# Kernel tuning notes

Hardware: AMD Instinct MI355X
Metric: run time of the kernel (lower is better)

Reference implementation:

```python
import jax, jax.numpy as jnp
import numpy as np

N_LEVELS = 16
N_FEATS = 2
MIN_RES = 16
MAX_RES = 2048
LOG2_T = 19
T = 1 << LOG2_T  # 524288 hash-table entries per level
B = np.exp((np.log(MAX_RES) - np.log(MIN_RES)) / (N_LEVELS - 1))  # per-level scale ~1.3819
PRIME_Y = np.uint32(2654435761)  # tcnn 2D spatial-hash prime (x prime is 1)
MASK = jnp.uint32(T - 1)


def hash_encode(uv, table):
    """Multiresolution hash-grid encoding (tcnn HashGrid, 2D, bilinear).
    uv: [N,2] in [0,1); table: [L,T,F]. Returns [N, L*F]."""
    outs = []
    for l in range(N_LEVELS):
        scale = MIN_RES * (B ** l) - 1.0          # tcnn grid_scale
        res = int(np.ceil(scale)) + 1             # tcnn grid_resolution
        dense = (res * res) <= T                  # small levels are dense grids
        pos = uv * jnp.float32(scale) + jnp.float32(0.5)
        pg_f = jnp.floor(pos)
        frac = pos - pg_f                          # [N,2] bilinear weights
        pg = pg_f.astype(jnp.uint32)

        def corner_idx(ox, oy):
            x = pg[:, 0] + jnp.uint32(ox)
            y = pg[:, 1] + jnp.uint32(oy)
            if dense:
                return (x + y * jnp.uint32(res)) & MASK
            return (x ^ (y * PRIME_Y)) & MASK

        fx = frac[:, 0:1]
        fy = frac[:, 1:2]
        tl = table[l]
        feat = ((1.0 - fx) * (1.0 - fy) * tl[corner_idx(0, 0)]
                + fx * (1.0 - fy) * tl[corner_idx(1, 0)]
                + (1.0 - fx) * fy * tl[corner_idx(0, 1)]
                + fx * fy * tl[corner_idx(1, 1)])
        outs.append(feat)
    return jnp.concatenate(outs, axis=-1)  # [N, 32]


def mlp(x, w0, w1, w2):
    # FullyFusedMLP: no biases, ReLU hidden, Sigmoid output
    h = jax.nn.relu(x @ w0)
    h = jax.nn.relu(h @ w1)
    return jax.nn.sigmoid(h @ w2)  # [N, 3]


def setup_inputs() -> dict:
    key = jax.random.key(0)
    ks = jax.random.split(key, 5)
    N = 2_097_152
    uv = jax.random.uniform(ks[0], (N, 2), jnp.float32)
    # tcnn HashGrid init: uniform in [-1e-4, 1e-4]
    table = jax.random.uniform(ks[1], (N_LEVELS, T, N_FEATS), jnp.float32, -1e-4, 1e-4)
    w0 = jax.random.normal(ks[2], (32, 64), jnp.float32) * jnp.float32(1.0 / np.sqrt(32))
    w1 = jax.random.normal(ks[3], (64, 64), jnp.float32) * jnp.float32(1.0 / np.sqrt(64))
    w2 = jax.random.normal(ks[4], (64, 3), jnp.float32) * jnp.float32(1.0 / np.sqrt(64))
    return {"uv": uv, "table": table, "w0": w0, "w1": w1, "w2": w2}


def reference(uv, table, w0, w1, w2):
    return mlp(hash_encode(uv, table), w0, w1, w2)
```

## Files before the change

### kernel.cpp

```cpp
#include <hip/hip_runtime.h>
#include <math.h>
#include <stdint.h>

#define NLV 16
#define LOG2T 19
#define TSZ (1u << LOG2T)
#define TMASK (TSZ - 1u)
#define PRIME_Y 2654435761u

#define WP8_BYTES  (4 * 64 * 8)
#define WP16_BYTES (10 * 64 * 16)
#define WPF_BYTES  (WP8_BYTES + WP16_BYTES)

#define FSCALE 8192.0f
#define FUNSCALE (1.0f / 8192.0f)

#define NCOARSE 512
#define P1_PTS 8192
#define P2_CAP 5120

struct NGPParams {
    float scale[NLV];
    unsigned res[NLV];
    unsigned hashed_mask;
};

struct __align__(8) pairld { float x, y, z, w; };

typedef __attribute__((ext_vector_type(8))) short bf16x8;
typedef __attribute__((ext_vector_type(4))) float f32x4;

__device__ inline ushort bf16_rn(float f) {
    uint32_t u = __float_as_uint(f);
    return (ushort)((u + 0x7FFFu + ((u >> 16) & 1u)) >> 16);
}
__device__ inline uint32_t pack_trunc(float a, float b) {
    return __builtin_amdgcn_perm(__float_as_uint(a), __float_as_uint(b), 0x07060302u);
}
__device__ inline ushort cvt_pk_fp8(float a, float b) {
    unsigned r = 0;
    asm("v_cvt_pk_fp8_f32 %0, %1, %2" : "+v"(r) : "v"(a), "v"(b));
    return (ushort)r;
}
__device__ inline unsigned coarse_of(float2 v) {
    unsigned b = (unsigned)(v.y * 512.f); return b > 511u ? 511u : b;
}
__device__ inline unsigned fine_of(float2 v) {
    unsigned b = (unsigned)(v.x * 256.f); return b > 255u ? 255u : b;
}
__device__ inline int xcd_swz(int orig, int nwg) {
    const int q = nwg >> 3, r = nwg & 7;
    const int xcd = orig & 7, k = orig >> 3;
    return (xcd < r ? xcd * (q + 1) : r * (q + 1) + (xcd - r) * q) + k;
}

__global__ __launch_bounds__(256) void ngp_prep_wfrag(
    const float* __restrict__ w0, const float* __restrict__ w1,
    const float* __restrict__ w2,
    unsigned long long* __restrict__ wp8, ushort* __restrict__ wp16,
    uint32_t* __restrict__ hist)
{
    const int t = threadIdx.x;
    hist[t] = 0; hist[t + 256] = 0;
    {
        const int f = t >> 6, lane = t & 63;
        const int g4 = lane >> 4, r16 = lane & 15;
        const int nn = f * 16 + r16, k0 = 8 * g4;
        float v[8];
        #pragma unroll
        for (int j = 0; j < 8; ++j) v[j] = w0[(k0 + j) * 64 + nn];
        const unsigned long long p0 = cvt_pk_fp8(v[0], v[1]);
        const unsigned long long p1 = cvt_pk_fp8(v[2], v[3]);
        const unsigned long long p2 = cvt_pk_fp8(v[4], v[5]);
        const unsigned long long p3 = cvt_pk_fp8(v[6], v[7]);
        wp8[f * 64 + lane] = p0 | (p1 << 16) | (p2 << 32) | (p3 << 48);
    }
    for (int i = 0; i < 3; ++i) {
        const int e = t + 256 * i;
        if (e >= 640) continue;
        const int f = e >> 6, lane = e & 63;
        const int g4 = lane >> 4, r16 = lane & 15;
        ushort v[8];
        if (f < 8) {
            const int nn = (f >> 1) * 16 + r16, k0 = (f & 1) * 32 + 8 * g4;
            #pragma unroll
            for (int j = 0; j < 8; ++j) v[j] = bf16_rn(w1[(k0 + j) * 64 + nn]);
        } else {
            const int nn = r16, k0 = (f - 8) * 32 + 8 * g4;
            #pragma unroll
            for (int j = 0; j < 8; ++j)
                v[j] = (nn < 3) ? bf16_rn(w2[(k0 + j) * 3 + nn]) : (ushort)0;
        }
        #pragma unroll
        for (int j = 0; j < 8; ++j) wp16[e * 8 + j] = v[j];
    }
}

__global__ __launch_bounds__(1024) void ngp_hist512(
    const float2* __restrict__ uv, uint32_t* __restrict__ hist, int n)
{
    __shared__ unsigned int h[NCOARSE];
    const int t = threadIdx.x;
    if (t < NCOARSE) h[t] = 0;
    __syncthreads();
    const int b0 = blockIdx.x * P1_PTS;
    #pragma unroll
    for (int k = 0; k < 8; ++k) {
        const int i = b0 + t + k * 1024;
        if (i < n) atomicAdd(&h[coarse_of(uv[i])], 1u);
    }
    __syncthreads();
    if (t < NCOARSE && h[t]) atomicAdd(&hist[t], h[t]);
}

__global__ __launch_bounds__(512) void ngp_scan512(
    const uint32_t* __restrict__ hist, uint32_t* __restrict__ base,
    uint32_t* __restrict__ cursor)
{
    __shared__ unsigned int s[NCOARSE];
    const int t = threadIdx.x;
    const uint32_t mine = hist[t];
    s[t] = mine;
    __syncthreads();
    for (int off = 1; off < NCOARSE; off <<= 1) {
        uint32_t v = (t >= off) ? s[t - off] : 0u;
        __syncthreads();
        s[t] += v;
        __syncthreads();
    }
    const uint32_t excl = s[t] - mine;
    base[t] = excl;
    cursor[t] = excl;
}

__global__ __launch_bounds__(1024) void ngp_pass1(
    const float2* __restrict__ uv, uint32_t* __restrict__ cursor,
    float2* __restrict__ suv, uint32_t* __restrict__ perm, int n)
{
    __shared__ float2       spt[P1_PTS];
    __shared__ unsigned int sid[P1_PTS];
    __shared__ unsigned int hist[NCOARSE], lbase[NCOARSE], lcur[NCOARSE], gbase[NCOARSE];
    __shared__ unsigned int stot;

    const int t = threadIdx.x;
    const int b0 = blockIdx.x * P1_PTS;
    if (t < NCOARSE) hist[t] = 0;
    __syncthreads();

    float2 p[8]; unsigned pc[8];
    #pragma unroll
    for (int k = 0; k < 8; ++k) {
        const int i = b0 + t + k * 1024;
        if (i < n) {
            p[k] = uv[i];
            pc[k] = coarse_of(p[k]);
            atomicAdd(&hist[pc[k]], 1u);
        } else pc[k] = 0xFFFFFFFFu;
    }
    __syncthreads();
    if (t < NCOARSE) lbase[t] = hist[t];
    __syncthreads();
    for (int off = 1; off < NCOARSE; off <<= 1) {
        uint32_t v = 0;
        if (t < NCOARSE && t >= off) v = lbase[t - off];
        __syncthreads();
        if (t < NCOARSE) lbase[t] += v;
        __syncthreads();
    }
    if (t < NCOARSE) {
        const uint32_t excl = lbase[t] - hist[t];
        lcur[t] = excl;
        gbase[t] = atomicAdd(&cursor[t], hist[t]);
        lbase[t] = excl;
        if (t == NCOARSE - 1) stot = excl + hist[t];
    }
    __syncthreads();
    #pragma unroll
    for (int k = 0; k < 8; ++k) {
        if (pc[k] != 0xFFFFFFFFu) {
            const uint32_t r = atomicAdd(&lcur[pc[k]], 1u);
            spt[r] = p[k];
            sid[r] = (unsigned)(b0 + t + k * 1024);
        }
    }
    __syncthreads();
    const uint32_t tot = stot;
    for (uint32_t j = t; j < tot; j += 1024) {
        const float2 v = spt[j];
        const unsigned c = coarse_of(v);
        const uint32_t d = gbase[c] + (j - lbase[c]);
        suv[d] = v;
        perm[d] = sid[j];
    }
}

__global__ __launch_bounds__(1024) void ngp_pass2(
    const uint32_t* __restrict__ basev, const uint32_t* __restrict__ histv,
    float2* __restrict__ suv, uint32_t* __restrict__ perm)
{
    __shared__ float2       spt[P2_CAP];
    __shared__ unsigned int sid[P2_CAP];
    __shared__ unsigned int hist[256], lbase[256], lcur[256];

    const int b = blockIdx.x;
    const uint32_t lo = basev[b];
    const uint32_t cnt = histv[b];
    if (cnt > P2_CAP) return;
    const int t = threadIdx.x;
    if (t < 256) hist[t] = 0;
    __syncthreads();
    for (uint32_t j = t; j < cnt; j += 1024) {
        const float2 v = suv[lo + j];
        spt[j] = v; sid[j] = perm[lo + j];
        atomicAdd(&hist[fine_of(v)], 1u);
    }
    __syncthreads();
    if (t < 256) lbase[t] = hist[t];
    __syncthreads();
    for (int off = 1; off < 256; off <<= 1) {
        uint32_t v = 0;
        if (t < 256 && t >= off) v = lbase[t - off];
        __syncthreads();
        if (t < 256) lbase[t] += v;
        __syncthreads();
    }
    if (t < 256) lcur[t] = lbase[t] - hist[t];
    __syncthreads();
    for (uint32_t j = t; j < cnt; j += 1024) {
        const float2 v = spt[j];
        const uint32_t r = atomicAdd(&lcur[fine_of(v)], 1u);
        suv[lo + r] = v;
        perm[lo + r] = sid[j];
    }
}

__global__ __launch_bounds__(256) void ngp_encode2_kernel(
    const float2* __restrict__ pts,
    const float2* __restrict__ table,
    ushort* __restrict__ xt,
    NGPParams p, int n, int chunks2)
{
    const int bid = blockIdx.x;
    const int pass = bid / chunks2;
    const int chunk = xcd_swz(bid - pass * chunks2, chunks2);
    const int base = chunk * 512 + threadIdx.x;

    float2 xy[2];
    #pragma unroll
    for (int q = 0; q < 2; ++q) {
        int idx = base + q * 256;
        xy[q] = pts[idx < n ? idx : (n - 1)];
    }

    const int l0 = (pass == 0) ? 0 : (pass == 1 ? 10 : 10 + pass);
    const int l1 = (pass == 0) ? 9 : (pass == 1 ? 11 : 10 + pass);

    for (int l = l0; l <= l1; ++l) {
        const float s = p.scale[l];
        const unsigned res = p.res[l];
        const bool hashed = (p.hashed_mask >> l) & 1u;
        const float2* tl = table + ((size_t)l << LOG2T);

        #pragma unroll
        for (int q = 0; q < 2; ++q) {
            const float px = xy[q].x * s + 0.5f;
            const float py = xy[q].y * s + 0.5f;
            const float fpx = floorf(px), fpy = floorf(py);
            const float fx = px - fpx, fy = py - fpy;
            const unsigned x0 = (unsigned)fpx, y0 = (unsigned)fpy;

            float2 c00, c10, c01, c11;
            if (!hashed) {
                const unsigned b0 = x0 + y0 * res;
                const pairld q0 = *(const pairld*)(tl + b0);
                const pairld q1 = *(const pairld*)(tl + b0 + res);
                c00 = make_float2(q0.x, q0.y); c10 = make_float2(q0.z, q0.w);
                c01 = make_float2(q1.x, q1.y); c11 = make_float2(q1.z, q1.w);
            } else {
                const unsigned hy0 = y0 * PRIME_Y;
                const unsigned hy1 = (y0 + 1u) * PRIME_Y;
                if (!(x0 & 1u)) {
                    const unsigned i0 = (x0 ^ hy0) & TMASK;
                    const unsigned i2 = (x0 ^ hy1) & TMASK;
                    const pairld q0 = *(const pairld*)(tl + (i0 & ~1u));
                    const pairld q2 = *(const pairld*)(tl + (i2 & ~1u));
                    if (i0 & 1u) { c00 = make_float2(q0.z, q0.w); c10 = make_float2(q0.x, q0.y); }
                    else         { c00 = make_float2(q0.x, q0.y); c10 = make_float2(q0.z, q0.w); }
                    if (i2 & 1u) { c01 = make_float2(q2.z, q2.w); c11 = make_float2(q2.x, q2.y); }
                    else         { c01 = make_float2(q2.x, q2.y); c11 = make_float2(q2.z, q2.w); }
                } else {
                    c00 = tl[(x0 ^ hy0) & TMASK];
                    c10 = tl[((x0 + 1u) ^ hy0) & TMASK];
                    c01 = tl[(x0 ^ hy1) & TMASK];
                    c11 = tl[((x0 + 1u) ^ hy1) & TMASK];
                }
            }

            const float w00 = (1.f - fx) * (1.f - fy);
            const float w10 = fx * (1.f - fy);
            const float w01 = (1.f - fx) * fy;
            const float w11 = fx * fy;
            const float f0 = w00 * c00.x + w10 * c10.x + w01 * c01.x + w11 * c11.x;
            const float f1 = w00 * c00.y + w10 * c10.y + w01 * c01.y + w11 * c11.y;
            const ushort pk = cvt_pk_fp8(f0 * FSCALE, f1 * FSCALE);
            const int idx = base + q * 256;
            if (idx < n) xt[(size_t)l * n + idx] = pk;
        }
    }
}

__global__ __launch_bounds__(256, 4) void ngp_mlp_persist(
    const ushort* __restrict__ xt,
    const unsigned long long* __restrict__ wp8,
    const ushort* __restrict__ wp16,
    const uint32_t* __restrict__ perm,
    float* __restrict__ out, int n, int nchunks)
{
    __shared__ __align__(16) ushort H[256 * 72];

    const int t = threadIdx.x;
    const int lane = t & 63;
    const int w = t >> 6;
    const int g4 = lane >> 4;
    const int r16 = lane & 15;

    unsigned long long wf8[4];
    #pragma unroll
    for (int f = 0; f < 4; ++f) wf8[f] = wp8[f * 64 + lane];
    bf16x8 wf16[10];
    #pragma unroll
    for (int f = 0; f < 10; ++f)
        wf16[f] = *(const bf16x8*)(wp16 + (size_t)(f * 64 + lane) * 8);

    for (int c = blockIdx.x; c < nchunks; c += gridDim.x) {
        const int pbase = c << 8;
        #pragma unroll
        for (int mi = 0; mi < 4; ++mi) {
            const int plocal = (w * 4 + mi) * 16 + r16;
            int pg = pbase + plocal;
            pg = pg < n ? pg : n - 1;
            union { ushort s[4]; unsigned long long v; } xv;
            #pragma unroll
            for (int c4 = 0; c4 < 4; ++c4)
                xv.s[c4] = xt[(size_t)(4 * g4 + c4) * n + pg];
            f32x4 a[4];
            #pragma unroll
            for (int nt = 0; nt < 4; ++nt)
                a[nt] = __builtin_amdgcn_mfma_f32_16x16x32_fp8_fp8(
                    (long)wf8[nt], (long)xv.v, (f32x4){0.f, 0.f, 0.f, 0.f}, 0, 0, 0);
            const int pl = plocal * 72;
            #pragma unroll
            for (int nt = 0; nt < 4; ++nt) {
                const uint32_t d0 = pack_trunc(fmaxf(a[nt][1] * FUNSCALE, 0.f),
                                               fmaxf(a[nt][0] * FUNSCALE, 0.f));
                const uint32_t d1 = pack_trunc(fmaxf(a[nt][3] * FUNSCALE, 0.f),
                                               fmaxf(a[nt][2] * FUNSCALE, 0.f));
                *(uint2*)&H[pl + nt * 16 + 4 * g4] = make_uint2(d0, d1);
            }
        }
        #pragma unroll
        for (int mi = 0; mi < 4; ++mi) {
            const int plocal = (w * 4 + mi) * 16 + r16;
            const int pl = plocal * 72;
            const bf16x8 bh0 = *(const bf16x8*)&H[pl + 8 * g4];
            const bf16x8 bh1 = *(const bf16x8*)&H[pl + 32 + 8 * g4];
            #pragma unroll
            for (int nt = 0; nt < 4; ++nt) {
                f32x4 acc = __builtin_amdgcn_mfma_f32_16x16x32_bf16(
                    wf16[nt * 2], bh0, (f32x4){0.f, 0.f, 0.f, 0.f}, 0, 0, 0);
                acc = __builtin_amdgcn_mfma_f32_16x16x32_bf16(
                    wf16[nt * 2 + 1], bh1, acc, 0, 0, 0);
                const uint32_t d0 = pack_trunc(fmaxf(acc[1], 0.f), fmaxf(acc[0], 0.f));
                const uint32_t d1 = pack_trunc(fmaxf(acc[3], 0.f), fmaxf(acc[2], 0.f));
                *(uint2*)&H[pl + nt * 16 + 4 * g4] = make_uint2(d0, d1);
            }
            const bf16x8 ch0 = *(const bf16x8*)&H[pl + 8 * g4];
            const bf16x8 ch1 = *(const bf16x8*)&H[pl + 32 + 8 * g4];
            f32x4 z = __builtin_amdgcn_mfma_f32_16x16x32_bf16(
                wf16[8], ch0, (f32x4){0.f, 0.f, 0.f, 0.f}, 0, 0, 0);
            z = __builtin_amdgcn_mfma_f32_16x16x32_bf16(wf16[9], ch1, z, 0, 0, 0);
            if (g4 == 0) {
                const int pgs = pbase + plocal;
                if (pgs < n) {
                    const int pg = perm ? (int)perm[pgs] : pgs;
                    #pragma unroll
                    for (int r = 0; r < 3; ++r)
                        out[(size_t)pg * 3 + r] = 1.f / (1.f + __expf(-z[r]));
                }
            }
        }
    }
}

__global__ __launch_bounds__(256) void ngp_fused_kernel(
    const float2* __restrict__ uv,
    const float2* __restrict__ table,
    const float4* __restrict__ w0,
    const float4* __restrict__ w1,
    const float*  __restrict__ w2,
    float* __restrict__ out,
    NGPParams p, int n)
{
    __shared__ float4 sw0[512];
    __shared__ float4 sw1[1024];
    __shared__ float  sw2[192];
    const int t = threadIdx.x;
    #pragma unroll
    for (int i = 0; i < 2; i++) sw0[t + 256 * i] = w0[t + 256 * i];
    #pragma unroll
    for (int i = 0; i < 4; i++) sw1[t + 256 * i] = w1[t + 256 * i];
    if (t < 192) sw2[t] = w2[t];
    __syncthreads();
    const int gi = blockIdx.x * 256 + t;
    if (gi >= n) return;
    const float2 xy = uv[gi];
    float feat[32];
    #pragma unroll
    for (int l = 0; l < NLV; l++) {
        const float s = p.scale[l];
        const unsigned res = p.res[l];
        const float px = xy.x * s + 0.5f;
        const float py = xy.y * s + 0.5f;
        const float fpx = floorf(px), fpy = floorf(py);
        const float fx = px - fpx, fy = py - fpy;
        const unsigned x0 = (unsigned)fpx, y0 = (unsigned)fpy;
        unsigned i00, i10, i01, i11;
        if (!((p.hashed_mask >> l) & 1u)) {
            const unsigned b = x0 + y0 * res;
            i00 = b & TMASK; i10 = (b + 1u) & TMASK;
            i01 = (b + res) & TMASK; i11 = (b + res + 1u) & TMASK;
        } else {
            const unsigned hy0 = y0 * PRIME_Y;
            const unsigned hy1 = (y0 + 1u) * PRIME_Y;
            i00 = (x0 ^ hy0) & TMASK; i10 = ((x0 + 1u) ^ hy0) & TMASK;
            i01 = (x0 ^ hy1) & TMASK; i11 = ((x0 + 1u) ^ hy1) & TMASK;
        }
        const float2* tl = table + ((size_t)l << LOG2T);
        const float2 c00 = tl[i00], c10 = tl[i10], c01 = tl[i01], c11 = tl[i11];
        const float w00 = (1.f - fx) * (1.f - fy);
        const float w10 = fx * (1.f - fy);
        const float w01 = (1.f - fx) * fy;
        const float w11 = fx * fy;
        feat[2 * l]     = w00 * c00.x + w10 * c10.x + w01 * c01.x + w11 * c11.x;
        feat[2 * l + 1] = w00 * c00.y + w10 * c10.y + w01 * c01.y + w11 * c11.y;
    }
    float2 h0[32];
    #pragma unroll
    for (int j = 0; j < 32; j++) h0[j] = make_float2(0.f, 0.f);
    #pragma unroll
    for (int k = 0; k < 32; k++) {
        const float f = feat[k];
        #pragma unroll
        for (int j = 0; j < 16; j++) {
            const float4 ww = sw0[k * 16 + j];
            h0[2 * j].x = fmaf(f, ww.x, h0[2 * j].x);
            h0[2 * j].y = fmaf(f, ww.y, h0[2 * j].y);
            h0[2 * j + 1].x = fmaf(f, ww.z, h0[2 * j + 1].x);
            h0[2 * j + 1].y = fmaf(f, ww.w, h0[2 * j + 1].y);
        }
    }
    #pragma unroll
    for (int j = 0; j < 32; j++) {
        h0[j].x = fmaxf(h0[j].x, 0.f);
        h0[j].y = fmaxf(h0[j].y, 0.f);
    }
    float2 h1[32];
    #pragma unroll
    for (int j = 0; j < 32; j++) h1[j] = make_float2(0.f, 0.f);
    #pragma unroll
    for (int k = 0; k < 64; k++) {
        const float f = (k & 1) ? h0[k >> 1].y : h0[k >> 1].x;
        #pragma unroll
        for (int j = 0; j < 16; j++) {
            const float4 ww = sw1[k * 16 + j];
            h1[2 * j].x = fmaf(f, ww.x, h1[2 * j].x);
            h1[2 * j].y = fmaf(f, ww.y, h1[2 * j].y);
            h1[2 * j + 1].x = fmaf(f, ww.z, h1[2 * j + 1].x);
            h1[2 * j + 1].y = fmaf(f, ww.w, h1[2 * j + 1].y);
        }
    }
    #pragma unroll
    for (int j = 0; j < 32; j++) {
        h1[j].x = fmaxf(h1[j].x, 0.f);
        h1[j].y = fmaxf(h1[j].y, 0.f);
    }
    float z0 = 0.f, z1 = 0.f, z2 = 0.f;
    #pragma unroll
    for (int k = 0; k < 64; k++) {
        const float f = (k & 1) ? h1[k >> 1].y : h1[k >> 1].x;
        z0 = fmaf(f, sw2[3 * k + 0], z0);
        z1 = fmaf(f, sw2[3 * k + 1], z1);
        z2 = fmaf(f, sw2[3 * k + 2], z2);
    }
    out[3 * gi + 0] = 1.f / (1.f + __expf(-z0));
    out[3 * gi + 1] = 1.f / (1.f + __expf(-z1));
    out[3 * gi + 2] = 1.f / (1.f + __expf(-z2));
}

extern "C" void kernel_launch(void* const* d_in, const int* in_sizes, int n_in,
                              void* d_out, int out_size, void* d_ws, size_t ws_size,
                              hipStream_t stream) {
    const float2* uv    = (const float2*)d_in[0];
    const float2* table = (const float2*)d_in[1];
    const float*  w0f   = (const float*)d_in[2];
    const float*  w1f   = (const float*)d_in[3];
    const float*  w2f   = (const float*)d_in[4];
    float* out = (float*)d_out;

    const int n = in_sizes[0] / 2;

    NGPParams p;
    p.hashed_mask = 0;
    const double B = exp((log(2048.0) - log(16.0)) / 15.0);
    for (int l = 0; l < NLV; l++) {
        const double scale = 16.0 * pow(B, (double)l) - 1.0;
        const long long res = (long long)ceil(scale) + 1;
        p.scale[l] = (float)scale;
        p.res[l] = (unsigned)res;
        if (res * res > (long long)TSZ) p.hashed_mask |= (1u << l);
    }

    const size_t xt_bytes   = (size_t)NLV * (size_t)n * 2u;
    const size_t wpf_bytes  = ((size_t)WPF_BYTES + 63u) & ~63ull;
    const size_t suv_bytes  = (size_t)n * 8u;
    const size_t perm_bytes = (size_t)n * 4u;
    const size_t ctl_bytes  = (size_t)NCOARSE * 4u * 3u;

    const size_t need_sorted = xt_bytes + wpf_bytes + suv_bytes + perm_bytes + ctl_bytes;
    const size_t need_plain  = xt_bytes + wpf_bytes;

    const int chunks  = (n + 255) / 256;
    const int chunks2 = (n + 511) / 512;

    if (ws_size < need_plain) {
        ngp_fused_kernel<<<chunks, 256, 0, stream>>>(
            uv, table, (const float4*)w0f, (const float4*)w1f, w2f, out, p, n);
        return;
    }

    ushort* xt = (ushort*)d_ws;
    unsigned long long* wp8 = (unsigned long long*)((char*)d_ws + xt_bytes);
    ushort* wp16 = (ushort*)((char*)d_ws + xt_bytes + WP8_BYTES);

    float2*   suv    = (float2*)((char*)d_ws + xt_bytes + wpf_bytes);
    uint32_t* perm   = (uint32_t*)((char*)suv + suv_bytes);
    uint32_t* hist   = (uint32_t*)((char*)perm + perm_bytes);
    uint32_t* basev  = hist + NCOARSE;
    uint32_t* cursor = basev + NCOARSE;

    const int mlp_blocks = chunks < 1024 ? chunks : 1024;

    if (ws_size < need_sorted) {
        ngp_prep_wfrag<<<1, 256, 0, stream>>>(w0f, w1f, w2f, wp8, wp16,
                                              (uint32_t*)((char*)d_ws + xt_bytes + WPF_BYTES - 2048));
        ngp_encode2_kernel<<<6 * chunks2, 256, 0, stream>>>(uv, table, xt, p, n, chunks2);
        ngp_mlp_persist<<<mlp_blocks, 256, 0, stream>>>(xt, wp8, wp16,
                                                        (const uint32_t*)nullptr, out, n, chunks);
        return;
    }

    const int p1_blocks = (n + P1_PTS - 1) / P1_PTS;

    ngp_prep_wfrag<<<1, 256, 0, stream>>>(w0f, w1f, w2f, wp8, wp16, hist);
    ngp_hist512<<<p1_blocks, 1024, 0, stream>>>(uv, hist, n);
    ngp_scan512<<<1, NCOARSE, 0, stream>>>(hist, basev, cursor);
    ngp_pass1<<<p1_blocks, 1024, 0, stream>>>(uv, cursor, suv, perm, n);
    ngp_pass2<<<NCOARSE, 1024, 0, stream>>>(basev, hist, suv, perm);
    ngp_encode2_kernel<<<6 * chunks2, 256, 0, stream>>>(suv, table, xt, p, n, chunks2);
    ngp_mlp_persist<<<mlp_blocks, 256, 0, stream>>>(xt, wp8, wp16, perm, out, n, chunks);
}
```

Before: 172.6 us.

## Fold global scan into sort passes and merge encode level passes

```diff
diff --git a/kernel.cpp b/kernel.cpp
--- a/kernel.cpp
+++ b/kernel.cpp
@@ -58,10 +58,10 @@
     const float* __restrict__ w0, const float* __restrict__ w1,
     const float* __restrict__ w2,
     unsigned long long* __restrict__ wp8, ushort* __restrict__ wp16,
-    uint32_t* __restrict__ hist)
+    uint32_t* __restrict__ ctl)
 {
     const int t = threadIdx.x;
-    hist[t] = 0; hist[t + 256] = 0;
+    if (ctl) { ctl[t] = 0; ctl[t + 256] = 0; ctl[t + 512] = 0; ctl[t + 768] = 0; }
     {
         const int f = t >> 6, lane = t & 63;
         const int g4 = lane >> 4, r16 = lane & 15;
@@ -113,38 +113,20 @@
     if (t < NCOARSE && h[t]) atomicAdd(&hist[t], h[t]);
 }
 
-__global__ __launch_bounds__(512) void ngp_scan512(
-    const uint32_t* __restrict__ hist, uint32_t* __restrict__ base,
-    uint32_t* __restrict__ cursor)
-{
-    __shared__ unsigned int s[NCOARSE];
-    const int t = threadIdx.x;
-    const uint32_t mine = hist[t];
-    s[t] = mine;
-    __syncthreads();
-    for (int off = 1; off < NCOARSE; off <<= 1) {
-        uint32_t v = (t >= off) ? s[t - off] : 0u;
-        __syncthreads();
-        s[t] += v;
-        __syncthreads();
-    }
-    const uint32_t excl = s[t] - mine;
-    base[t] = excl;
-    cursor[t] = excl;
-}
-
 __global__ __launch_bounds__(1024) void ngp_pass1(
-    const float2* __restrict__ uv, uint32_t* __restrict__ cursor,
+    const float2* __restrict__ uv, const uint32_t* __restrict__ ghist,
+    uint32_t* __restrict__ cursor,
     float2* __restrict__ suv, uint32_t* __restrict__ perm, int n)
 {
     __shared__ float2       spt[P1_PTS];
     __shared__ unsigned int sid[P1_PTS];
-    __shared__ unsigned int hist[NCOARSE], lbase[NCOARSE], lcur[NCOARSE], gbase[NCOARSE];
+    __shared__ unsigned int h[NCOARSE], lbase[NCOARSE], lcur[NCOARSE];
+    __shared__ unsigned int gex[NCOARSE], gbase[NCOARSE];
     __shared__ unsigned int stot;
 
     const int t = threadIdx.x;
     const int b0 = blockIdx.x * P1_PTS;
-    if (t < NCOARSE) hist[t] = 0;
+    if (t < NCOARSE) h[t] = 0;
     __syncthreads();
 
     float2 p[8]; unsigned pc[8];
@@ -154,25 +136,29 @@
         if (i < n) {
             p[k] = uv[i];
             pc[k] = coarse_of(p[k]);
-            atomicAdd(&hist[pc[k]], 1u);
+            atomicAdd(&h[pc[k]], 1u);
         } else pc[k] = 0xFFFFFFFFu;
     }
     __syncthreads();
-    if (t < NCOARSE) lbase[t] = hist[t];
+    unsigned mg = 0, ml = 0;
+    if (t < NCOARSE) {
+        mg = ghist[t]; ml = h[t];
+        gex[t] = mg; lbase[t] = ml;
+    }
     __syncthreads();
     for (int off = 1; off < NCOARSE; off <<= 1) {
-        uint32_t v = 0;
-        if (t < NCOARSE && t >= off) v = lbase[t - off];
+        unsigned vg = 0, vl = 0;
+        if (t < NCOARSE && t >= off) { vg = gex[t - off]; vl = lbase[t - off]; }
         __syncthreads();
-        if (t < NCOARSE) lbase[t] += v;
+        if (t < NCOARSE) { gex[t] += vg; lbase[t] += vl; }
         __syncthreads();
     }
     if (t < NCOARSE) {
-        const uint32_t excl = lbase[t] - hist[t];
-        lcur[t] = excl;
-        gbase[t] = atomicAdd(&cursor[t], hist[t]);
-        lbase[t] = excl;
-        if (t == NCOARSE - 1) stot = excl + hist[t];
+        const unsigned lex = lbase[t] - ml;
+        lcur[t] = lex;
+        gbase[t] = (gex[t] - mg) + atomicAdd(&cursor[t], ml);
+        lbase[t] = lex;
+        if (t == NCOARSE - 1) stot = lex + ml;
     }
     __syncthreads();
     #pragma unroll
@@ -195,27 +181,41 @@
 }
 
 __global__ __launch_bounds__(1024) void ngp_pass2(
-    const uint32_t* __restrict__ basev, const uint32_t* __restrict__ histv,
+    const uint32_t* __restrict__ ghist,
     float2* __restrict__ suv, uint32_t* __restrict__ perm)
 {
     __shared__ float2       spt[P2_CAP];
     __shared__ unsigned int sid[P2_CAP];
-    __shared__ unsigned int hist[256], lbase[256], lcur[256];
-
+    __shared__ unsigned int gex[NCOARSE];
+    __shared__ unsigned int h[256], lbase[256], lcur[256];
+    __shared__ unsigned int s_lo, s_cnt;
+
+    const int t = threadIdx.x;
     const int b = blockIdx.x;
-    const uint32_t lo = basev[b];
-    const uint32_t cnt = histv[b];
+    unsigned mine = 0;
+    if (t < NCOARSE) { mine = ghist[t]; gex[t] = mine; }
+    __syncthreads();
+    for (int off = 1; off < NCOARSE; off <<= 1) {
+        unsigned v = 0;
+        if (t < NCOARSE && t >= off) v = gex[t - off];
+        __syncthreads();
+        if (t < NCOARSE) gex[t] += v;
+        __syncthreads();
+    }
+    if (t == b) { s_cnt = mine; s_lo = gex[b] - mine; }
+    __syncthreads();
+    const uint32_t lo = s_lo;
+    const uint32_t cnt = s_cnt;
     if (cnt > P2_CAP) return;
-    const int t = threadIdx.x;
-    if (t < 256) hist[t] = 0;
+    if (t < 256) h[t] = 0;
     __syncthreads();
     for (uint32_t j = t; j < cnt; j += 1024) {
         const float2 v = suv[lo + j];
         spt[j] = v; sid[j] = perm[lo + j];
-        atomicAdd(&hist[fine_of(v)], 1u);
-    }
-    __syncthreads();
-    if (t < 256) lbase[t] = hist[t];
+        atomicAdd(&h[fine_of(v)], 1u);
+    }
+    __syncthreads();
+    if (t < 256) lbase[t] = h[t];
     __syncthreads();
     for (int off = 1; off < 256; off <<= 1) {
         uint32_t v = 0;
@@ -224,7 +224,7 @@
         if (t < 256) lbase[t] += v;
         __syncthreads();
     }
-    if (t < 256) lcur[t] = lbase[t] - hist[t];
+    if (t < 256) lcur[t] = lbase[t] - h[t];
     __syncthreads();
     for (uint32_t j = t; j < cnt; j += 1024) {
         const float2 v = spt[j];
@@ -252,8 +252,8 @@
         xy[q] = pts[idx < n ? idx : (n - 1)];
     }
 
-    const int l0 = (pass == 0) ? 0 : (pass == 1 ? 10 : 10 + pass);
-    const int l1 = (pass == 0) ? 9 : (pass == 1 ? 11 : 10 + pass);
+    const int l0 = (pass == 0) ? 0 : 11 + pass;
+    const int l1 = (pass == 0) ? 11 : 11 + pass;
 
     for (int l = l0; l <= l1; ++l) {
         const float s = p.scale[l];
@@ -524,7 +524,7 @@
     const size_t wpf_bytes  = ((size_t)WPF_BYTES + 63u) & ~63ull;
     const size_t suv_bytes  = (size_t)n * 8u;
     const size_t perm_bytes = (size_t)n * 4u;
-    const size_t ctl_bytes  = (size_t)NCOARSE * 4u * 3u;
+    const size_t ctl_bytes  = (size_t)NCOARSE * 4u * 2u;
 
     const size_t need_sorted = xt_bytes + wpf_bytes + suv_bytes + perm_bytes + ctl_bytes;
     const size_t need_plain  = xt_bytes + wpf_bytes;
@@ -545,15 +545,14 @@
     float2*   suv    = (float2*)((char*)d_ws + xt_bytes + wpf_bytes);
     uint32_t* perm   = (uint32_t*)((char*)suv + suv_bytes);
     uint32_t* hist   = (uint32_t*)((char*)perm + perm_bytes);
-    uint32_t* basev  = hist + NCOARSE;
-    uint32_t* cursor = basev + NCOARSE;
+    uint32_t* cursor = hist + NCOARSE;
 
     const int mlp_blocks = chunks < 1024 ? chunks : 1024;
 
     if (ws_size < need_sorted) {
         ngp_prep_wfrag<<<1, 256, 0, stream>>>(w0f, w1f, w2f, wp8, wp16,
-                                              (uint32_t*)((char*)d_ws + xt_bytes + WPF_BYTES - 2048));
-        ngp_encode2_kernel<<<6 * chunks2, 256, 0, stream>>>(uv, table, xt, p, n, chunks2);
+                                              (uint32_t*)nullptr);
+        ngp_encode2_kernel<<<5 * chunks2, 256, 0, stream>>>(uv, table, xt, p, n, chunks2);
         ngp_mlp_persist<<<mlp_blocks, 256, 0, stream>>>(xt, wp8, wp16,
                                                         (const uint32_t*)nullptr, out, n, chunks);
         return;
@@ -563,9 +562,8 @@
 
     ngp_prep_wfrag<<<1, 256, 0, stream>>>(w0f, w1f, w2f, wp8, wp16, hist);
     ngp_hist512<<<p1_blocks, 1024, 0, stream>>>(uv, hist, n);
-    ngp_scan512<<<1, NCOARSE, 0, stream>>>(hist, basev, cursor);
-    ngp_pass1<<<p1_blocks, 1024, 0, stream>>>(uv, cursor, suv, perm, n);
-    ngp_pass2<<<NCOARSE, 1024, 0, stream>>>(basev, hist, suv, perm);
-    ngp_encode2_kernel<<<6 * chunks2, 256, 0, stream>>>(suv, table, xt, p, n, chunks2);
+    ngp_pass1<<<p1_blocks, 1024, 0, stream>>>(uv, hist, cursor, suv, perm, n);
+    ngp_pass2<<<NCOARSE, 1024, 0, stream>>>(hist, suv, perm);
+    ngp_encode2_kernel<<<5 * chunks2, 256, 0, stream>>>(suv, table, xt, p, n, chunks2);
     ngp_mlp_persist<<<mlp_blocks, 256, 0, stream>>>(xt, wp8, wp16, perm, out, n, chunks);
 }
```

Measured after the change: 170.4 us. No clear change (-1.3%).
